# Kernel tuning notes

Hardware: AMD Instinct MI355X
Metric: run time of the kernel (lower is better)

Reference implementation:

```python
import jax, jax.numpy as jnp
import numpy as np

T, B, S = 32, 64, 64          # tgt_len, batch, src_len
V, E, H, L = 32000, 512, 1024, 2  # vocab, word_vec, rnn_size, layers


def setup_inputs() -> dict:
    key = jax.random.key(0)
    ks = jax.random.split(key, 16)
    s = 0.02
    emb = jax.random.normal(ks[5], (V, E)) * s
    emb = emb.at[0].set(0.0)  # padding_idx=0 row is zero
    return {
        "input": jax.random.randint(ks[0], (T, B), 0, V),
        "h0": jax.random.normal(ks[1], (L, B, H)) * s,
        "c0": jax.random.normal(ks[2], (L, B, H)) * s,
        "context": jax.random.normal(ks[3], (S, B, H)),
        "init_output": jax.random.normal(ks[4], (B, H)) * s,
        "embedding": emb,
        "W_ih0": jax.random.normal(ks[6], (4 * H, E + H)) * s,  # layer0 input = emb + input-feed
        "W_hh0": jax.random.normal(ks[7], (4 * H, H)) * s,
        "b0": jnp.zeros((4 * H,), jnp.float32),
        "W_ih1": jax.random.normal(ks[8], (4 * H, H)) * s,
        "W_hh1": jax.random.normal(ks[9], (4 * H, H)) * s,
        "b1": jnp.zeros((4 * H,), jnp.float32),
        "attn_in_w": jax.random.normal(ks[10], (H, H)) * s,
        "attn_out_w": jax.random.normal(ks[11], (H, 2 * H)) * s,
        "copy_in_w": jax.random.normal(ks[12], (H, H)) * s,
    }


def _lstm_cell(x, h, c, W_ih, W_hh, b):
    g = x @ W_ih.T + h @ W_hh.T + b
    i, f, gg, o = jnp.split(g, 4, axis=-1)  # PyTorch gate order i,f,g,o
    c_new = jax.nn.sigmoid(f) * c + jax.nn.sigmoid(i) * jnp.tanh(gg)
    h_new = jax.nn.sigmoid(o) * jnp.tanh(c_new)
    return h_new, c_new


def _global_attention(in_w, out_w, query, ctx):
    # query: (B,H), ctx: (B,S,H)
    q = query @ in_w.T
    scores = jnp.einsum('bd,bsd->bs', q, ctx)
    a = jax.nn.softmax(scores, axis=-1)
    wctx = jnp.einsum('bs,bsd->bd', a, ctx)
    out = jnp.tanh(jnp.concatenate([wctx, query], axis=-1) @ out_w.T)
    return out, a


def reference(input, h0, c0, context, init_output, embedding,
              W_ih0, W_hh0, b0, W_ih1, W_hh1, b1,
              attn_in_w, attn_out_w, copy_in_w):
    ctx = jnp.transpose(context, (1, 0, 2))  # (B,S,H)
    emb = embedding[input]                    # (T,B,E)

    def step(carry, emb_t):
        h, c, out_feed = carry
        x = jnp.concatenate([emb_t, out_feed], axis=-1)  # input feed
        h0n, c0n = _lstm_cell(x, h[0], c[0], W_ih0, W_hh0, b0)
        h1n, c1n = _lstm_cell(h0n, h[1], c[1], W_ih1, W_hh1, b1)
        out, a_std = _global_attention(attn_in_w, attn_out_w, h1n, ctx)
        # copy attention: only the weights are kept by the original module
        qc = out @ copy_in_w.T
        a_copy = jax.nn.softmax(jnp.einsum('bd,bsd->bs', qc, ctx), axis=-1)
        new_carry = (jnp.stack([h0n, h1n]), jnp.stack([c0n, c1n]), out)
        return new_carry, (out, a_std, a_copy)

    (h_T, c_T, _), (outputs, attn_std, attn_copy) = jax.lax.scan(
        step, (h0, c0, init_output), emb)
    return outputs, (h_T, c_T), attn_std, attn_copy
```

## Files before the change

### kernel.cpp

```cpp
#include <hip/hip_runtime.h>

typedef unsigned short u16;
typedef unsigned int   u32;
typedef __attribute__((ext_vector_type(8))) __bf16 bfrag;
typedef __attribute__((ext_vector_type(4))) float  f32x4;
typedef __attribute__((ext_vector_type(2))) u32    u32x2;
typedef __attribute__((ext_vector_type(4))) u32    u32x4;

#define DEVI static __device__ __forceinline__

#define ST2SC(p, v)    asm volatile("global_store_short %0, %1, off sc0 sc1"   :: "v"(p), "v"(v) : "memory")
#define ST4SC(p, v)    asm volatile("global_store_dword %0, %1, off sc0 sc1"   :: "v"(p), "v"(v) : "memory")
#define ST8SC(p, v)    asm volatile("global_store_dwordx2 %0, %1, off sc0 sc1" :: "v"(p), "v"(v) : "memory")
#define ST16SC(p, v)   asm volatile("global_store_dwordx4 %0, %1, off sc0 sc1" :: "v"(p), "v"(v) : "memory")
#define VMFLUSH()      asm volatile("s_waitcnt vmcnt(0)" ::: "memory")

constexpr long OUT_OFF = 0;
constexpr long HT_OFF  = 2097152;
constexpr long CT_OFF  = 2228224;
constexpr long AS_OFF  = 2359296;
constexpr long AC_OFF  = 2490368;

constexpr long WAO_O   = 0;
constexpr long CTX_O   = 4194304;
constexpr long OFR_O   = 0;
constexpr long H0R_O   = 4194304;
constexpr long H1R_O   = 8388608;
constexpr long WAI_O   = 12582912;
constexpr long WC_O    = 14680064;
constexpr long CTXW_O  = 16777216;
constexpr long CTXWC_O = 25165824;
constexpr long CTXOT_O = 33554432;
constexpr long EBF_O   = 41943040;
constexpr long OF0_O   = 44040192;
constexpr long H00_O   = 44171264;
constexpr long H10_O   = 44302336;
constexpr long AB_O    = 44433408;
constexpr long AFLAG_O = 44957696;
constexpr long BAR_O   = 44965888;

constexpr int W0LDS_O = 0;
constexpr int W1LDS_O = 81920;
constexpr int SCR_O   = 147456;
constexpr int SCR2_O  = 156160;

struct KParams {
  const int* input; const float* h0; const float* c0; const float* context;
  const float* init_output; const float* embedding;
  const float* W_ih0; const float* W_hh0; const float* b0;
  const float* W_ih1; const float* W_hh1; const float* b1;
  const float* attn_in; const float* attn_out; const float* copy_in;
  float* out; char* ws;
};

DEVI float bf2f(u16 u) { u32 x = ((u32)u) << 16; return __builtin_bit_cast(float, x); }
DEVI u16 f2bf(float f) {
  u32 x = __builtin_bit_cast(u32, f);
  u32 r = x + 0x7fffu + ((x >> 16) & 1u);
  return (u16)(r >> 16);
}
DEVI void cvtc_sc(const float* s, char* d) {
  float4 v = *(const float4*)s;
  u32x2 u;
  u[0] = (u32)f2bf(v.x) | ((u32)f2bf(v.y) << 16);
  u[1] = (u32)f2bf(v.z) | ((u32)f2bf(v.w) << 16);
  ST8SC(d, u);
}
DEVI float sigm(float x)  { return 1.f / (1.f + __expf(-x)); }
DEVI float tanh_(float x) { return 1.f - 2.f / (__expf(2.f * x) + 1.f); }
DEVI f32x4 mfma16(bfrag a, bfrag b, f32x4 c) {
  return __builtin_amdgcn_mfma_f32_16x16x32_bf16(a, b, c, 0, 0, 0);
}
DEVI u32 fragoff(int m, int k) {
  return (u32)((((k >> 5) * 4 + (m >> 4)) * 64 + ((k >> 3) & 3) * 16 + (m & 15)) * 16 + (k & 7) * 2);
}
DEVI char* of_slot(char* w, int s) { return w + (s ? OFR_O + (long)(s - 1) * 131072 : OF0_O); }
DEVI char* h0_slot(char* w, int s) { return w + (s ? H0R_O + (long)(s - 1) * 131072 : H00_O); }
DEVI char* h1_slot(char* w, int s) { return w + (s ? H1R_O + (long)(s - 1) * 131072 : H10_O); }

DEVI void pollflags(u32* flags, u32 gen) {
  int t = threadIdx.x;
  for (;;) {
    u32 a = __hip_atomic_load(&flags[t],       __ATOMIC_RELAXED, __HIP_MEMORY_SCOPE_AGENT);
    u32 b = __hip_atomic_load(&flags[64 + t],  __ATOMIC_RELAXED, __HIP_MEMORY_SCOPE_AGENT);
    u32 c = __hip_atomic_load(&flags[128 + t], __ATOMIC_RELAXED, __HIP_MEMORY_SCOPE_AGENT);
    u32 d = __hip_atomic_load(&flags[192 + t], __ATOMIC_RELAXED, __HIP_MEMORY_SCOPE_AGENT);
    if (__all((a >= gen) && (b >= gen) && (c >= gen) && (d >= gen))) break;
    __builtin_amdgcn_s_sleep(1);
  }
}
DEVI void barr_arrive(u32* flags, u32 gen) {
  VMFLUSH();
  __syncthreads();
  if (threadIdx.x == 0)
    __hip_atomic_store(&flags[blockIdx.x], gen, __ATOMIC_RELAXED, __HIP_MEMORY_SCOPE_AGENT);
}
DEVI void barr_wait(u32* flags, u32 gen) {
  u32* bc = flags + 320;
  if (blockIdx.x == 128) {
    if (threadIdx.x < 64) pollflags(flags, gen);
    __syncthreads();
    if (threadIdx.x == 0)
      __hip_atomic_store(bc, gen, __ATOMIC_RELAXED, __HIP_MEMORY_SCOPE_AGENT);
  } else {
    if (threadIdx.x == 0) {
      while (__hip_atomic_load(bc, __ATOMIC_RELAXED, __HIP_MEMORY_SCOPE_AGENT) < gen)
        __builtin_amdgcn_s_sleep(1);
    }
  }
  __syncthreads();
  asm volatile("" ::: "memory");
}
DEVI void gsync_fence(u32* flags, u32 gen) {
  __syncthreads();
  if (threadIdx.x == 0) {
    __builtin_amdgcn_fence(__ATOMIC_RELEASE, "agent");
    __hip_atomic_store(&flags[blockIdx.x], gen, __ATOMIC_RELAXED, __HIP_MEMORY_SCOPE_AGENT);
  }
  if (threadIdx.x < 64) pollflags(flags, gen);
  if (threadIdx.x == 0) __builtin_amdgcn_fence(__ATOMIC_ACQUIRE, "agent");
  __syncthreads();
}

template<int N4>
DEVI void gseg(f32x4& acc, const char* Af, int kkA0, int mt, int lane,
               const char* W, int wRowK, int kkW0, int brow, int ke) {
  const u32 sw = (u32)((brow & 7) << 4);
#pragma unroll
  for (int g = 0; g < N4; ++g) {
#pragma unroll
    for (int q = 0; q < 4; ++q) {
      const char* pa = Af + ((((kkA0 + g * 4 + q) * 4 + mt) * 64 + lane) << 4);
      bfrag av = *(const bfrag*)pa;
      int kkW = kkW0 + g * 4 + q;
      u32 off = ((u32)(brow * wRowK + kkW * 32 + ke) * 2) ^ sw;
      acc = mfma16(av, *(const bfrag*)(W + off), acc);
    }
  }
}

DEVI void scr_store(float* scr, int slot, f32x4 acc) {
  const int lane = threadIdx.x & 63;
#pragma unroll
  for (int r = 0; r < 4; ++r)
    scr[slot * 272 + ((lane >> 4) * 4 + r) * 17 + (lane & 15)] = acc[r];
}

DEVI void pointwise64(int bid, const float* scr, const float* bias, float (&cst)[4], char* hfrag) {
  const int m = threadIdx.x;
  const int mt = m >> 4, ml = m & 15;
  u32 hp0 = 0, hp1 = 0;
#pragma unroll
  for (int u = 0; u < 4; ++u) {
    const int j = bid * 4 + u;
    float g0 = scr[(mt*2)*272 + ml*17 + u]      + scr[(mt*2+1)*272 + ml*17 + u]      + bias[j];
    float g1 = scr[(mt*2)*272 + ml*17 + 4 + u]  + scr[(mt*2+1)*272 + ml*17 + 4 + u]  + bias[1024 + j];
    float g2 = scr[(mt*2)*272 + ml*17 + 8 + u]  + scr[(mt*2+1)*272 + ml*17 + 8 + u]  + bias[2048 + j];
    float g3 = scr[(mt*2)*272 + ml*17 + 12 + u] + scr[(mt*2+1)*272 + ml*17 + 12 + u] + bias[3072 + j];
    float cn = sigm(g1) * cst[u] + sigm(g0) * tanh_(g2);
    cst[u] = cn;
    u32 hb = (u32)f2bf(sigm(g3) * tanh_(cn));
    if (u == 0) hp0 = hb; else if (u == 1) hp0 |= hb << 16;
    else if (u == 2) hp1 = hb; else hp1 |= hb << 16;
  }
  u32x2 v; v[0] = hp0; v[1] = hp1;
  ST8SC(hfrag + fragoff(m, bid * 4), v);
}

DEVI void ctxw_gemm(int mt, const u16* Ctx, const u16* Wm, u16* dst) {
  const int tid = threadIdx.x, lane = tid & 63, w = tid >> 6;
  const int arow = mt * 16 + (lane & 15);
  const int ke = (lane >> 4) * 8;
#pragma unroll
  for (int i = 0; i < 8; ++i) {
    int nt = w * 8 + i;
    const u16* A = Ctx + (long)arow * 1024 + ke;
    const u16* B = Wm + (long)(nt * 16 + (lane & 15)) * 1024 + ke;
    f32x4 acc = {0.f, 0.f, 0.f, 0.f};
    for (int kk = 0; kk < 1024; kk += 32)
      acc = mfma16(*(const bfrag*)(A + kk), *(const bfrag*)(B + kk), acc);
#pragma unroll
    for (int r = 0; r < 4; ++r)
      ST2SC((char*)(dst + (long)(mt * 16 + (lane >> 4) * 4 + r) * 1024 + nt * 16 + (lane & 15)),
            (u32)f2bf(acc[r]));
  }
}

DEVI void ctxo_gemm(int bid, const u16* Ctx, const u16* Wao, u16* dst) {
  const int tid = threadIdx.x, lane = tid & 63, w = tid >> 6;
  const int arow = bid * 16 + (lane & 15);
  const int ke = (lane >> 4) * 8;
  const int b = bid >> 2, s0 = (bid & 3) * 16 + (lane >> 4) * 4;
#pragma unroll
  for (int i = 0; i < 8; ++i) {
    int nt = w * 8 + i;
    int j = nt * 16 + (lane & 15);
    const u16* A = Ctx + (long)arow * 1024 + ke;
    const u16* B = Wao + (long)j * 2048 + ke;
    f32x4 acc = {0.f, 0.f, 0.f, 0.f};
    for (int kk = 0; kk < 1024; kk += 32)
      acc = mfma16(*(const bfrag*)(A + kk), *(const bfrag*)(B + kk), acc);
    u32x2 q;
    q[0] = (u32)f2bf(acc[0]) | ((u32)f2bf(acc[1]) << 16);
    q[1] = (u32)f2bf(acc[2]) | ((u32)f2bf(acc[3]) << 16);
    ST8SC((char*)(dst + ((long)(b * 1024 + j) * 64 + s0)), q);
  }
}

__global__ __launch_bounds__(512, 1) void decoder_kernel(KParams p) {
  extern __shared__ char smem[];
  char*  W0   = smem + W0LDS_O;
  char*  W1   = smem + W1LDS_O;
  float* scr  = (float*)(smem + SCR_O);
  float* scr2 = (float*)(smem + SCR2_O);

  char* wsb = p.ws;
  u16* Wao   = (u16*)(wsb + WAO_O);
  u16* Wai   = (u16*)(wsb + WAI_O);
  u16* Wc    = (u16*)(wsb + WC_O);
  u16* Ctx   = (u16*)(wsb + CTX_O);
  u16* CtxW  = (u16*)(wsb + CTXW_O);
  u16* CtxWc = (u16*)(wsb + CTXWC_O);
  u16* CtxOT = (u16*)(wsb + CTXOT_O);
  u32* bar   = (u32*)(wsb + BAR_O);

  const int bid = blockIdx.x, tid = threadIdx.x;
  const int lane = tid & 63, w = tid >> 6;
  const long gtid = (long)bid * 512 + tid, NT = 256l * 512;
  u32 gen = 1;

  {
    float* tile = (float*)smem;
    for (int pass = 0; pass < 2; ++pass) {
      const float* src = pass ? p.copy_in : p.attn_in;
      u16* dst = pass ? Wc : Wai;
      int tr = bid >> 4, tc = bid & 15;
      {
        int r = tid >> 3, c = (tid & 7) * 8;
        const float4* s4 = (const float4*)(src + (long)(tr * 64 + r) * 1024 + tc * 64 + c);
        float4 a = s4[0], b = s4[1];
        float* tp = tile + r * 69 + c;
        tp[0] = a.x; tp[1] = a.y; tp[2] = a.z; tp[3] = a.w;
        tp[4] = b.x; tp[5] = b.y; tp[6] = b.z; tp[7] = b.w;
      }
      __syncthreads();
      {
        int r2 = tid >> 3, c2 = (tid & 7) * 8;
        u32x4 q;
#pragma unroll
        for (int i = 0; i < 4; ++i) {
          float lo = tile[(c2 + 2 * i) * 69 + r2];
          float hi = tile[(c2 + 2 * i + 1) * 69 + r2];
          q[i] = (u32)f2bf(lo) | ((u32)f2bf(hi) << 16);
        }
        ST16SC((char*)(dst + (long)(tc * 64 + r2) * 1024 + tr * 64 + c2), q);
      }
      __syncthreads();
    }
  }

  for (int i = tid; i < 5120; i += 512) {
    int row = i / 320, k = (i % 320) * 8;
    int R = (row >> 2) * 1024 + bid * 4 + (row & 3);
    const float* src = (k < 1536) ? (p.W_ih0 + (long)R * 1536 + k)
                                  : (p.W_hh0 + (long)R * 1024 + (k - 1536));
    float4 a = *(const float4*)src, b = *(const float4*)(src + 4);
    uint4 q;
    q.x = (u32)f2bf(a.x) | ((u32)f2bf(a.y) << 16);
    q.y = (u32)f2bf(a.z) | ((u32)f2bf(a.w) << 16);
    q.z = (u32)f2bf(b.x) | ((u32)f2bf(b.y) << 16);
    q.w = (u32)f2bf(b.z) | ((u32)f2bf(b.w) << 16);
    u32 off = ((u32)(row * 2560 + k) * 2) ^ ((u32)((row & 7) << 4));
    *(uint4*)(W0 + off) = q;
  }
  for (int i = tid; i < 4096; i += 512) {
    int row = i / 256, k = (i % 256) * 8;
    int R = (row >> 2) * 1024 + bid * 4 + (row & 3);
    const float* src = (k < 1024) ? (p.W_ih1 + (long)R * 1024 + k)
                                  : (p.W_hh1 + (long)R * 1024 + (k - 1024));
    float4 a = *(const float4*)src, b = *(const float4*)(src + 4);
    uint4 q;
    q.x = (u32)f2bf(a.x) | ((u32)f2bf(a.y) << 16);
    q.y = (u32)f2bf(a.z) | ((u32)f2bf(a.w) << 16);
    q.z = (u32)f2bf(b.x) | ((u32)f2bf(b.y) << 16);
    q.w = (u32)f2bf(b.z) | ((u32)f2bf(b.w) << 16);
    u32 off = ((u32)(row * 2048 + k) * 2) ^ ((u32)((row & 7) << 4));
    *(uint4*)(W1 + off) = q;
  }

  for (long i = gtid; i < 524288; i += NT) cvtc_sc(p.attn_out + i * 4, (char*)(Wao + i * 4));
  for (long i = gtid; i < 1048576; i += NT) {
    long b = i >> 14, s = (i >> 8) & 63, kq = i & 255;
    cvtc_sc(p.context + ((s * 64 + b) * 1024 + kq * 4), (char*)(Ctx + i * 4));
  }
  for (long i = gtid; i < 262144; i += NT) {
    long row = i >> 7; long t = row >> 6, b = row & 63;
    long k0 = (i & 127) * 4;
    long tok = p.input[row];
    cvtc_sc(p.embedding + tok * 512 + k0, wsb + EBF_O + t * 65536 + fragoff((int)b, (int)k0));
  }
  for (long i = gtid; i < 16384; i += NT) {
    long b = i >> 8, k0 = (i & 255) * 4;
    cvtc_sc(p.init_output + i * 4, of_slot(wsb, 0) + fragoff((int)b, (int)k0));
  }
  for (long i = gtid; i < 32768; i += NT) {
    long l = i >> 14, rem = i & 16383, b = rem >> 8, k0 = (rem & 255) * 4;
    cvtc_sc(p.h0 + i * 4, (l ? h1_slot(wsb, 0) : h0_slot(wsb, 0)) + fragoff((int)b, (int)k0));
  }

  float cR0[4] = {0.f, 0.f, 0.f, 0.f}, cR1[4] = {0.f, 0.f, 0.f, 0.f};
  if (tid < 64) {
#pragma unroll
    for (int u = 0; u < 4; ++u) {
      cR0[u] = p.c0[(long)tid * 1024 + bid * 4 + u];
      cR1[u] = p.c0[65536 + (long)tid * 1024 + bid * 4 + u];
    }
  }

  gsync_fence(bar, gen); ++gen;

  ctxw_gemm(bid, Ctx, Wai, CtxW);
  ctxw_gemm(bid, Ctx, Wc, CtxWc);
  ctxo_gemm(bid, Ctx, Wao, CtxOT);
  gsync_fence(bar, gen); ++gen;

  const int xcd = bid & 7, idx = bid >> 3;
  const int ntP4 = xcd * 8 + (idx & 7), mtP4 = idx >> 3;
  const int browP4 = ntP4 * 16 + (lane & 15);
  const int ke_ = (lane >> 4) * 8;
  bfrag waoreg[4];
#pragma unroll
  for (int q = 0; q < 4; ++q)
    waoreg[q] = *(const bfrag*)(Wao + (long)browP4 * 2048 + 1024 + (w * 4 + q) * 32 + ke_);

  const int mt_ = w & 3, kh_ = w >> 2;
  const int brow_ = lane & 15;

  f32x4 accP1 = {0.f, 0.f, 0.f, 0.f}, accP2;
  {
    const char* E0  = wsb + EBF_O;
    const char* H0p = h0_slot(wsb, 0);
    if (kh_ == 0) {
      gseg<2>(accP1, E0,  0,  mt_, lane, W0, 2560, 0,  brow_, ke_);
      gseg<4>(accP1, H0p, 0,  mt_, lane, W0, 2560, 48, brow_, ke_);
    } else {
      gseg<2>(accP1, E0,  8,  mt_, lane, W0, 2560, 8,  brow_, ke_);
      gseg<4>(accP1, H0p, 16, mt_, lane, W0, 2560, 64, brow_, ke_);
    }
  }

  for (int t = 0; t < 32; ++t) {
    const char* OFc   = of_slot(wsb, t);
    char*       Hb0cF = h0_slot(wsb, t + 1);
    char*       Hb1cF = h1_slot(wsb, t + 1);
    const char* Hb1pF = h1_slot(wsb, t);
    char*       ABt   = wsb + AB_O + (long)t * 16384;

    {
      f32x4 acc = accP1;
      if (kh_ == 0) gseg<4>(acc, OFc, 0,  mt_, lane, W0, 2560, 16, brow_, ke_);
      else          gseg<4>(acc, OFc, 16, mt_, lane, W0, 2560, 32, brow_, ke_);
      scr_store(scr, mt_ * 2 + kh_, acc);
      __syncthreads();
      if (tid < 64) pointwise64(bid, scr, p.b0, cR0, Hb0cF);
    }
    barr_arrive(bar, gen);
    accP2 = f32x4{0.f, 0.f, 0.f, 0.f};
    if (kh_ == 0) gseg<4>(accP2, Hb1pF, 0,  mt_, lane, W1, 2048, 32, brow_, ke_);
    else          gseg<4>(accP2, Hb1pF, 16, mt_, lane, W1, 2048, 48, brow_, ke_);
    barr_wait(bar, gen); ++gen;

    {
      f32x4 acc = accP2;
      if (kh_ == 0) gseg<4>(acc, Hb0cF, 0,  mt_, lane, W1, 2048, 0,  brow_, ke_);
      else          gseg<4>(acc, Hb0cF, 16, mt_, lane, W1, 2048, 16, brow_, ke_);
      scr_store(scr, mt_ * 2 + kh_, acc);
      __syncthreads();
      if (tid < 64) pointwise64(bid, scr, p.b1, cR1, Hb1cF);
    }
    barr_arrive(bar, gen);
    accP1 = f32x4{0.f, 0.f, 0.f, 0.f};
    {
      const char* En = wsb + EBF_O + (long)((t + 1) & 31) * 65536;
      if (kh_ == 0) {
        gseg<2>(accP1, En,    0,  mt_, lane, W0, 2560, 0,  brow_, ke_);
        gseg<2>(accP1, Hb0cF, 0,  mt_, lane, W0, 2560, 48, brow_, ke_);
      } else {
        gseg<2>(accP1, En,    8,  mt_, lane, W0, 2560, 8,  brow_, ke_);
        gseg<2>(accP1, Hb0cF, 16, mt_, lane, W0, 2560, 64, brow_, ke_);
      }
    }
    barr_wait(bar, gen); ++gen;

    if (bid < 64) {
      const int b = bid;
      float h1v[16];
      {
        int k0 = lane * 16;
        const u32* hp0 = (const u32*)(Hb1cF + fragoff(b, k0));
        const u32* hp1 = (const u32*)(Hb1cF + fragoff(b, k0 + 8));
        u32 uu[8] = {hp0[0], hp0[1], hp0[2], hp0[3], hp1[0], hp1[1], hp1[2], hp1[3]};
#pragma unroll
        for (int i = 0; i < 8; ++i) {
          h1v[2 * i]     = bf2f((u16)(uu[i] & 0xffff));
          h1v[2 * i + 1] = bf2f((u16)(uu[i] >> 16));
        }
      }
      const u16* cwb = CtxW + (long)b * 65536;
#pragma unroll
      for (int si = 0; si < 8; ++si) {
        int s = w * 8 + si;
        const u32* u = (const u32*)(cwb + (long)s * 1024 + lane * 16);
        float acc = 0.f;
#pragma unroll
        for (int i = 0; i < 8; ++i) {
          u32 x = u[i];
          acc += h1v[2 * i] * bf2f((u16)(x & 0xffff));
          acc += h1v[2 * i + 1] * bf2f((u16)(x >> 16));
        }
#pragma unroll
        for (int off = 32; off; off >>= 1) acc += __shfl_down(acc, off, 64);
        if (lane == 0) scr2[s] = acc;
      }
      __syncthreads();
      if (w == 0) {
        float v = scr2[lane];
        float mx = v;
#pragma unroll
        for (int off = 32; off; off >>= 1) mx = fmaxf(mx, __shfl_xor(mx, off, 64));
        float e = __expf(v - mx);
        float sm = e;
#pragma unroll
        for (int off = 32; off; off >>= 1) sm += __shfl_xor(sm, off, 64);
        float a = e / sm;
        ST4SC(ABt + (u32)(b * 64 + lane) * 4, __builtin_bit_cast(u32, a));
        ST4SC((char*)(p.out + AS_OFF + (long)t * 4096 + b * 64 + lane), __builtin_bit_cast(u32, a));
        VMFLUSH();
        if (lane == 0)
          ST4SC(wsb + AFLAG_O + ((u32)t * 64 + b) * 4, 1u);
      }
    }
    {
      const char* bp = Hb1cF;
      bfrag h0_ = *(const bfrag*)(bp + ((((w * 4 + 0) * 4 + mtP4) * 64 + lane) << 4));
      bfrag h1_ = *(const bfrag*)(bp + ((((w * 4 + 1) * 4 + mtP4) * 64 + lane) << 4));
      bfrag h2_ = *(const bfrag*)(bp + ((((w * 4 + 2) * 4 + mtP4) * 64 + lane) << 4));
      bfrag h3_ = *(const bfrag*)(bp + ((((w * 4 + 3) * 4 + mtP4) * 64 + lane) << 4));
      f32x4 a4 = {0.f, 0.f, 0.f, 0.f};
      a4 = mfma16(h0_, waoreg[0], a4);
      a4 = mfma16(h1_, waoreg[1], a4);
      a4 = mfma16(h2_, waoreg[2], a4);
      a4 = mfma16(h3_, waoreg[3], a4);
      scr_store(scr, w, a4);
    }

    {
      if (tid < 16) {
        const u32* fp = (const u32*)(wsb + AFLAG_O + ((u32)t * 64 + mtP4 * 16 + tid) * 4);
        while (__hip_atomic_load(fp, __ATOMIC_RELAXED, __HIP_MEMORY_SCOPE_AGENT) == 0)
          __builtin_amdgcn_s_sleep(1);
      }
      __syncthreads();
      {
        int b0i = tid >> 6, s0i = tid & 63;
        int b1i = (tid + 512) >> 6;
        scr2[tid]       = *(const float*)(ABt + (u32)(((mtP4 * 16 + b0i) * 64 + s0i)) * 4);
        scr2[tid + 512] = *(const float*)(ABt + (u32)(((mtP4 * 16 + b1i) * 64 + s0i)) * 4);
      }
      __syncthreads();
      const int pair = tid >> 1, half = tid & 1;
      const int m_l = pair >> 4, j_l = pair & 15;
      const int b = mtP4 * 16 + m_l, j = ntP4 * 16 + j_l;
      const u32* cp = (const u32*)(CtxOT + ((long)(b * 1024 + j) * 64 + half * 32));
      const float* al = scr2 + m_l * 64 + half * 32;
      float acc = 0.f;
#pragma unroll
      for (int i = 0; i < 16; ++i) {
        u32 x = cp[i];
        acc += al[2 * i] * bf2f((u16)(x & 0xffff));
        acc += al[2 * i + 1] * bf2f((u16)(x >> 16));
      }
      float v = acc + __shfl_xor(acc, 1, 64);
      if (half == 0) {
        float h1p = 0.f;
#pragma unroll
        for (int q = 0; q < 8; ++q) h1p += scr[q * 272 + m_l * 17 + j_l];
        v = tanh_(v + h1p);
        ST4SC((char*)(p.out + (long)t * 65536 + b * 1024 + j), __builtin_bit_cast(u32, v));
        u32 hv = (u32)f2bf(v);
        ST2SC(of_slot(wsb, t + 1) + fragoff(b, j), hv);
      }
    }
    barr_arrive(bar, gen);
    if (kh_ == 0) gseg<2>(accP1, Hb0cF, 8,  mt_, lane, W0, 2560, 56, brow_, ke_);
    else          gseg<2>(accP1, Hb0cF, 24, mt_, lane, W0, 2560, 72, brow_, ke_);
    barr_wait(bar, gen); ++gen;
  }

  if (tid < 64) {
#pragma unroll
    for (int u = 0; u < 4; ++u) {
      int j = bid * 4 + u;
      p.out[CT_OFF + (long)tid * 1024 + j]         = cR0[u];
      p.out[CT_OFF + 65536 + (long)tid * 1024 + j] = cR1[u];
    }
  }
  if (tid < 256) {
    int u = tid >> 6, m = tid & 63, j = bid * 4 + u;
    u16 a0 = *(const u16*)(h0_slot(wsb, 32) + fragoff(m, j));
    u16 a1 = *(const u16*)(h1_slot(wsb, 32) + fragoff(m, j));
    p.out[HT_OFF + (long)m * 1024 + j]         = bf2f(a0);
    p.out[HT_OFF + 65536 + (long)m * 1024 + j] = bf2f(a1);
  }

  if (bid < 64) {
    const int b = bid;
    u16* cw = (u16*)smem;
    __syncthreads();
    {
      const uint4* src = (const uint4*)(CtxWc + (long)b * 65536);
      uint4* dst = (uint4*)cw;
      for (int i = tid; i < 8192; i += 512) dst[i] = src[i];
    }
    __syncthreads();
    float* lds_s = scr;
    for (int t = 0; t < 32; ++t) {
      float ov[16];
      {
        const float4* op = (const float4*)(p.out + (long)t * 65536 + b * 1024 + lane * 16);
#pragma unroll
        for (int i = 0; i < 4; ++i) {
          float4 v = op[i];
          ov[4 * i] = v.x; ov[4 * i + 1] = v.y; ov[4 * i + 2] = v.z; ov[4 * i + 3] = v.w;
        }
      }
#pragma unroll
      for (int si = 0; si < 8; ++si) {
        int s = w * 8 + si;
        const u32* u = (const u32*)(cw + s * 1024 + lane * 16);
        float acc = 0.f;
#pragma unroll
        for (int i = 0; i < 8; ++i) {
          u32 x = u[i];
          acc += ov[2 * i] * bf2f((u16)(x & 0xffff));
          acc += ov[2 * i + 1] * bf2f((u16)(x >> 16));
        }
#pragma unroll
        for (int off = 32; off; off >>= 1) acc += __shfl_down(acc, off, 64);
        if (lane == 0) lds_s[s] = acc;
      }
      __syncthreads();
      if (w == 0) {
        float v = lds_s[lane];
        float mx = v;
#pragma unroll
        for (int off = 32; off; off >>= 1) mx = fmaxf(mx, __shfl_xor(mx, off, 64));
        float e = __expf(v - mx);
        float sm = e;
#pragma unroll
        for (int off = 32; off; off >>= 1) sm += __shfl_xor(sm, off, 64);
        p.out[AC_OFF + (long)t * 4096 + b * 64 + lane] = e / sm;
      }
      __syncthreads();
    }
  }
}

extern "C" void kernel_launch(void* const* d_in, const int* in_sizes, int n_in,
                              void* d_out, int out_size, void* d_ws, size_t ws_size,
                              hipStream_t stream) {
  KParams p;
  p.input       = (const int*)d_in[0];
  p.h0          = (const float*)d_in[1];
  p.c0          = (const float*)d_in[2];
  p.context     = (const float*)d_in[3];
  p.init_output = (const float*)d_in[4];
  p.embedding   = (const float*)d_in[5];
  p.W_ih0       = (const float*)d_in[6];
  p.W_hh0       = (const float*)d_in[7];
  p.b0          = (const float*)d_in[8];
  p.W_ih1       = (const float*)d_in[9];
  p.W_hh1       = (const float*)d_in[10];
  p.b1          = (const float*)d_in[11];
  p.attn_in     = (const float*)d_in[12];
  p.attn_out    = (const float*)d_in[13];
  p.copy_in     = (const float*)d_in[14];
  p.out         = (float*)d_out;
  p.ws          = (char*)d_ws;

  (void)hipFuncSetAttribute((const void*)decoder_kernel,
                            hipFuncAttributeMaxDynamicSharedMemorySize, 160256);
  (void)hipMemsetAsync((char*)d_ws + AB_O, 0, 534528, stream);
  void* args[] = { &p };
  (void)hipLaunchCooperativeKernel((void*)decoder_kernel, dim3(256), dim3(512),
                                   args, 160256, stream);
}
```

Measured before the change: 1.631 ms.

## Overlap copy-attention with recurrence steps and drop sleep in spin-waits

The copy-attention softmax used to run as a serial tail phase after all 32 steps, on blocks 0-63. It now runs one step behind inside the main time loop on blocks 192-255, with only the final step left after the loop. The ctx·W values are read straight from global memory instead of being staged into LDS. Two smaller changes ride along: s_sleep is removed from the barrier and flag spin loops to cut wake-up latency, and the CtxOT loads are hoisted ahead of the attention-flag wait. Risks are extra per-step work on some blocks, which can lengthen the critical path between grid barriers, and more memory traffic from busy polling.

```diff
diff --git a/kernel.cpp b/kernel.cpp
--- a/kernel.cpp
+++ b/kernel.cpp
@@ -86,7 +86,6 @@
     u32 c = __hip_atomic_load(&flags[128 + t], __ATOMIC_RELAXED, __HIP_MEMORY_SCOPE_AGENT);
     u32 d = __hip_atomic_load(&flags[192 + t], __ATOMIC_RELAXED, __HIP_MEMORY_SCOPE_AGENT);
     if (__all((a >= gen) && (b >= gen) && (c >= gen) && (d >= gen))) break;
-    __builtin_amdgcn_s_sleep(1);
   }
 }
 DEVI void barr_arrive(u32* flags, u32 gen) {
@@ -104,8 +103,7 @@
       __hip_atomic_store(bc, gen, __ATOMIC_RELAXED, __HIP_MEMORY_SCOPE_AGENT);
   } else {
     if (threadIdx.x == 0) {
-      while (__hip_atomic_load(bc, __ATOMIC_RELAXED, __HIP_MEMORY_SCOPE_AGENT) < gen)
-        __builtin_amdgcn_s_sleep(1);
+      while (__hip_atomic_load(bc, __ATOMIC_RELAXED, __HIP_MEMORY_SCOPE_AGENT) < gen) {}
     }
   }
   __syncthreads();
@@ -165,6 +163,48 @@
   }
   u32x2 v; v[0] = hp0; v[1] = hp1;
   ST8SC(hfrag + fragoff(m, bid * 4), v);
+}
+
+DEVI void copyattn_step(int b, int tau, const u16* CtxWc, const float* outp,
+                        float* xch, float* dout) {
+  const int tid = threadIdx.x, lane = tid & 63, w = tid >> 6;
+  float ov[16];
+  {
+    const float4* op = (const float4*)(outp + (long)tau * 65536 + b * 1024 + lane * 16);
+#pragma unroll
+    for (int i = 0; i < 4; ++i) {
+      float4 v = op[i];
+      ov[4 * i] = v.x; ov[4 * i + 1] = v.y; ov[4 * i + 2] = v.z; ov[4 * i + 3] = v.w;
+    }
+  }
+  const u16* cwb = CtxWc + (long)b * 65536;
+#pragma unroll
+  for (int si = 0; si < 8; ++si) {
+    int s = w * 8 + si;
+    const u32* u = (const u32*)(cwb + (long)s * 1024 + lane * 16);
+    float acc = 0.f;
+#pragma unroll
+    for (int i = 0; i < 8; ++i) {
+      u32 x = u[i];
+      acc += ov[2 * i] * bf2f((u16)(x & 0xffff));
+      acc += ov[2 * i + 1] * bf2f((u16)(x >> 16));
+    }
+#pragma unroll
+    for (int off = 32; off; off >>= 1) acc += __shfl_down(acc, off, 64);
+    if (lane == 0) xch[s] = acc;
+  }
+  __syncthreads();
+  if (w == 0) {
+    float v = xch[lane];
+    float mx = v;
+#pragma unroll
+    for (int off = 32; off; off >>= 1) mx = fmaxf(mx, __shfl_xor(mx, off, 64));
+    float e = __expf(v - mx);
+    float sm = e;
+#pragma unroll
+    for (int off = 32; off; off >>= 1) sm += __shfl_xor(sm, off, 64);
+    dout[AC_OFF + (long)tau * 4096 + b * 64 + lane] = e / sm;
+  }
 }
 
 DEVI void ctxw_gemm(int mt, const u16* Ctx, const u16* Wm, u16* dst) {
@@ -439,6 +479,7 @@
         if (lane == 0)
           ST4SC(wsb + AFLAG_O + ((u32)t * 64 + b) * 4, 1u);
       }
+      __syncthreads();
     }
     {
       const char* bp = Hb1cF;
@@ -453,12 +494,22 @@
       a4 = mfma16(h3_, waoreg[3], a4);
       scr_store(scr, w, a4);
     }
+    if (bid >= 192 && t > 0)
+      copyattn_step(bid - 192, t - 1, CtxWc, p.out, scr2, p.out);
 
     {
+      const int pair = tid >> 1, half = tid & 1;
+      const int m_l = pair >> 4, j_l = pair & 15;
+      const int b = mtP4 * 16 + m_l, j = ntP4 * 16 + j_l;
+      u32 cpr[16];
+      {
+        const u32* cp = (const u32*)(CtxOT + ((long)(b * 1024 + j) * 64 + half * 32));
+#pragma unroll
+        for (int i = 0; i < 16; ++i) cpr[i] = cp[i];
+      }
       if (tid < 16) {
         const u32* fp = (const u32*)(wsb + AFLAG_O + ((u32)t * 64 + mtP4 * 16 + tid) * 4);
-        while (__hip_atomic_load(fp, __ATOMIC_RELAXED, __HIP_MEMORY_SCOPE_AGENT) == 0)
-          __builtin_amdgcn_s_sleep(1);
+        while (__hip_atomic_load(fp, __ATOMIC_RELAXED, __HIP_MEMORY_SCOPE_AGENT) == 0) {}
       }
       __syncthreads();
       {
@@ -468,15 +519,11 @@
         scr2[tid + 512] = *(const float*)(ABt + (u32)(((mtP4 * 16 + b1i) * 64 + s0i)) * 4);
       }
       __syncthreads();
-      const int pair = tid >> 1, half = tid & 1;
-      const int m_l = pair >> 4, j_l = pair & 15;
-      const int b = mtP4 * 16 + m_l, j = ntP4 * 16 + j_l;
-      const u32* cp = (const u32*)(CtxOT + ((long)(b * 1024 + j) * 64 + half * 32));
       const float* al = scr2 + m_l * 64 + half * 32;
       float acc = 0.f;
 #pragma unroll
       for (int i = 0; i < 16; ++i) {
-        u32 x = cp[i];
+        u32 x = cpr[i];
         acc += al[2 * i] * bf2f((u16)(x & 0xffff));
         acc += al[2 * i + 1] * bf2f((u16)(x >> 16));
       }
@@ -513,56 +560,9 @@
     p.out[HT_OFF + 65536 + (long)m * 1024 + j] = bf2f(a1);
   }
 
-  if (bid < 64) {
-    const int b = bid;
-    u16* cw = (u16*)smem;
+  if (bid >= 192) {
     __syncthreads();
-    {
-      const uint4* src = (const uint4*)(CtxWc + (long)b * 65536);
-      uint4* dst = (uint4*)cw;
-      for (int i = tid; i < 8192; i += 512) dst[i] = src[i];
-    }
-    __syncthreads();
-    float* lds_s = scr;
-    for (int t = 0; t < 32; ++t) {
-      float ov[16];
-      {
-        const float4* op = (const float4*)(p.out + (long)t * 65536 + b * 1024 + lane * 16);
-#pragma unroll
-        for (int i = 0; i < 4; ++i) {
-          float4 v = op[i];
-          ov[4 * i] = v.x; ov[4 * i + 1] = v.y; ov[4 * i + 2] = v.z; ov[4 * i + 3] = v.w;
-        }
-      }
-#pragma unroll
-      for (int si = 0; si < 8; ++si) {
-        int s = w * 8 + si;
-        const u32* u = (const u32*)(cw + s * 1024 + lane * 16);
-        float acc = 0.f;
-#pragma unroll
-        for (int i = 0; i < 8; ++i) {
-          u32 x = u[i];
-          acc += ov[2 * i] * bf2f((u16)(x & 0xffff));
-          acc += ov[2 * i + 1] * bf2f((u16)(x >> 16));
-        }
-#pragma unroll
-        for (int off = 32; off; off >>= 1) acc += __shfl_down(acc, off, 64);
-        if (lane == 0) lds_s[s] = acc;
-      }
-      __syncthreads();
-      if (w == 0) {
-        float v = lds_s[lane];
-        float mx = v;
-#pragma unroll
-        for (int off = 32; off; off >>= 1) mx = fmaxf(mx, __shfl_xor(mx, off, 64));
-        float e = __expf(v - mx);
-        float sm = e;
-#pragma unroll
-        for (int off = 32; off; off >>= 1) sm += __shfl_xor(sm, off, 64);
-        p.out[AC_OFF + (long)t * 4096 + b * 64 + lane] = e / sm;
-      }
-      __syncthreads();
-    }
+    copyattn_step(bid - 192, 31, CtxWc, p.out, scr2, p.out);
   }
 }
 
```

New measurement: 1.534 ms. 5.9% less time.
